# Kernel tuning notes

Hardware: AMD Instinct MI355X
Metric: run time of the kernel (lower is better)

## Reference

```python
import jax, jax.numpy as jnp
import numpy as np

S = 2048      # sequence length
E = 2048      # n_embd
H = 16        # n_head
D = E // H    # head_dim = 128
EPS = 1e-5


def _layer_norm(x, w):
    # eqx.nn.LayerNorm, use_bias=False: (x - mean) / sqrt(var + eps) * w
    mu = jnp.mean(x, axis=-1, keepdims=True)
    var = jnp.mean(jnp.square(x - mu), axis=-1, keepdims=True)
    return (x - mu) * jax.lax.rsqrt(var + EPS) * w


def setup_inputs() -> dict:
    key = jax.random.key(0)
    ks = jax.random.split(key, 7)
    x = jax.random.normal(ks[0], (S, E), dtype=jnp.float32)
    # equinox Linear weights are (out_features, in_features); y = W @ x
    w_attn = jax.random.normal(ks[1], (3 * E, E), dtype=jnp.float32) * 0.02
    w_proj_attn = jax.random.normal(ks[2], (E, E), dtype=jnp.float32) * 0.02
    w_fc = jax.random.normal(ks[3], (4 * E, E), dtype=jnp.float32) * 0.02
    w_proj_ffn = jax.random.normal(ks[4], (E, 4 * E), dtype=jnp.float32) * 0.02
    ln1_w = jnp.ones((E,), dtype=jnp.float32)
    ln2_w = jnp.ones((E,), dtype=jnp.float32)
    return {"x": x, "ln1_w": ln1_w, "ln2_w": ln2_w, "w_attn": w_attn,
            "w_proj_attn": w_proj_attn, "w_fc": w_fc, "w_proj_ffn": w_proj_ffn}


def reference(x, ln1_w, ln2_w, w_attn, w_proj_attn, w_fc, w_proj_ffn):
    # --- LN1 + fused QKV projection ---
    h = _layer_norm(x, ln1_w)                       # [S, E]
    qkv = h @ w_attn.T                              # [S, 3E]
    q, k, v = jnp.split(qkv, 3, axis=-1)
    q = q.reshape(S, H, D)
    k = k.reshape(S, H, D)
    v = v.reshape(S, H, D)
    # --- naive causal attention with materialized [H, S, T] scores ---
    scale = 1.0 / jnp.sqrt(jnp.float32(D))
    causal_bias = (jnp.arange(S)[:, None] < jnp.arange(S)[None, :]) * (-10000.0)
    scores = jnp.einsum('shd,thd->hst', q, k) * scale + causal_bias  # [H,S,T]
    probs = jax.nn.softmax(scores, axis=-1)
    attn = jnp.einsum('hst,thd->shd', probs, v).reshape(S, E)
    x = x + attn @ w_proj_attn.T
    # --- LN2 + GELU MLP ---
    h2 = _layer_norm(x, ln2_w)                      # [S, E]
    f = jax.nn.gelu(h2 @ w_fc.T) @ w_proj_ffn.T    # [S,4E] -> [S,E]
    return x + f
```

## Files before the change

### kernel.cpp

```cpp
#include <hip/hip_runtime.h>
#include <hip/hip_bf16.h>

#define S_LEN 2048
#define EMB   2048
#define NH    16
#define HD    128

typedef __bf16 bf16x8 __attribute__((ext_vector_type(8)));
typedef __bf16 bf16x4 __attribute__((ext_vector_type(4)));
typedef float  f32x4  __attribute__((ext_vector_type(4)));
typedef short  s16x4  __attribute__((ext_vector_type(4)));

__device__ __forceinline__ void async_copy16(void* lds, const void* g) {
  __builtin_amdgcn_global_load_lds((__attribute__((address_space(1))) void*)(void*)g,
                                   (__attribute__((address_space(3))) void*)lds, 16, 0, 0);
}

__device__ __forceinline__ unsigned lds_addr(const void* p) {
  return (unsigned)(uintptr_t)(const __attribute__((address_space(3))) char*)p;
}

__device__ __forceinline__ s16x4 tr16(unsigned addr) {
  s16x4 d;
  asm volatile("ds_read_b64_tr_b16 %0, %1" : "=v"(d) : "v"(addr));
  return d;
}

__device__ __forceinline__ float gelu_tanh(float x) {
  float x3 = x * x * x;
  float t  = 0.7978845608028654f * (x + 0.044715f * x3);
  float th = 1.0f - 2.0f / (__expf(2.0f * t) + 1.0f);
  return 0.5f * x * (1.0f + th);
}

__global__ __launch_bounds__(256) void cast_kernel(const float* __restrict__ in,
                                                   __bf16* __restrict__ out, int n) {
  int i = (blockIdx.x * 256 + threadIdx.x) * 4;
  if (i >= n) return;
  float4 v = *(const float4*)(in + i);
  bf16x4 o;
  o[0] = (__bf16)v.x; o[1] = (__bf16)v.y; o[2] = (__bf16)v.z; o[3] = (__bf16)v.w;
  *(bf16x4*)(out + i) = o;
}

__global__ __launch_bounds__(256) void ln_kernel(const float* __restrict__ x,
                                                 const float* __restrict__ w,
                                                 __bf16* __restrict__ out) {
  int row = blockIdx.x;
  int t = threadIdx.x;
  const float* xr = x + (size_t)row * EMB;
  float4 a = *(const float4*)(xr + t * 8);
  float4 b = *(const float4*)(xr + t * 8 + 4);
  float s  = a.x + a.y + a.z + a.w + b.x + b.y + b.z + b.w;
  float sq = a.x*a.x + a.y*a.y + a.z*a.z + a.w*a.w + b.x*b.x + b.y*b.y + b.z*b.z + b.w*b.w;
  #pragma unroll
  for (int o = 32; o > 0; o >>= 1) { s += __shfl_xor(s, o); sq += __shfl_xor(sq, o); }
  __shared__ float red[8];
  if ((t & 63) == 0) { red[t >> 6] = s; red[(t >> 6) + 4] = sq; }
  __syncthreads();
  s  = red[0] + red[1] + red[2] + red[3];
  sq = red[4] + red[5] + red[6] + red[7];
  float mu  = s * (1.0f / EMB);
  float var = sq * (1.0f / EMB) - mu * mu;
  float rs  = rsqrtf(var + 1e-5f);
  float4 w1 = *(const float4*)(w + t * 8);
  float4 w2 = *(const float4*)(w + t * 8 + 4);
  bf16x8 ov;
  ov[0] = (__bf16)((a.x - mu) * rs * w1.x);
  ov[1] = (__bf16)((a.y - mu) * rs * w1.y);
  ov[2] = (__bf16)((a.z - mu) * rs * w1.z);
  ov[3] = (__bf16)((a.w - mu) * rs * w1.w);
  ov[4] = (__bf16)((b.x - mu) * rs * w2.x);
  ov[5] = (__bf16)((b.y - mu) * rs * w2.y);
  ov[6] = (__bf16)((b.z - mu) * rs * w2.z);
  ov[7] = (__bf16)((b.w - mu) * rs * w2.w);
  *(bf16x8*)(out + (size_t)row * EMB + t * 8) = ov;
}

#define GPHASE(KH, MG, LOADB, STAGE_CALL, VMWAIT)                                           \
  {                                                                                         \
    if (LOADB) {                                                                            \
      _Pragma("unroll")                                                                     \
      for (int n = 0; n < 4; n++) {                                                         \
        int row = wc * 64 + n * 16 + fr;                                                    \
        b[n] = *(const bf16x8*)&Bs[((p * 2 + (KH)) * 256 + row) * 32 + ((g ^ (fr & 3)) << 3)]; \
      }                                                                                     \
    }                                                                                       \
    _Pragma("unroll")                                                                       \
    for (int m = 0; m < 4; m++) {                                                           \
      int row = wr * 128 + ((MG) * 4 + m) * 16 + fr;                                        \
      a[m] = *(const bf16x8*)&As[((p * 2 + (KH)) * 256 + row) * 32 + ((g ^ (fr & 3)) << 3)];   \
    }                                                                                       \
    STAGE_CALL;                                                                             \
    __builtin_amdgcn_sched_barrier(0);                                                      \
    __builtin_amdgcn_s_setprio(1);                                                          \
    _Pragma("unroll")                                                                       \
    for (int m = 0; m < 4; m++)                                                             \
      _Pragma("unroll")                                                                     \
      for (int n = 0; n < 4; n++)                                                           \
        acc[(MG) * 4 + m][n] =                                                              \
            __builtin_amdgcn_mfma_f32_16x16x32_bf16(a[m], b[n], acc[(MG) * 4 + m][n], 0, 0, 0); \
    __builtin_amdgcn_s_setprio(0);                                                          \
    VMWAIT;                                                                                 \
    __builtin_amdgcn_s_barrier();                                                           \
  }

template <int EPI>
__global__ __launch_bounds__(512, 2) void gemm256(const __bf16* __restrict__ A,
                                                  const __bf16* __restrict__ B,
                                                  void* __restrict__ Cv,
                                                  int M, int N, int K, int Ksl, int NN) {
  __shared__ __bf16 As[2 * 2 * 256 * 32];
  __shared__ __bf16 Bs[2 * 2 * 256 * 32];

  const int t = threadIdx.x, w = t >> 6, l = t & 63;
  const int fr = l & 15, g = l >> 4;
  const int wr = w >> 2, wc = w & 3;

  const int nwg = gridDim.x;
  const int wg = (blockIdx.x & 7) * (nwg >> 3) + (blockIdx.x >> 3);
  const int NMN = (M >> 8) * NN;
  const int z = wg / NMN, rr = wg - z * NMN;
  const int my = rr / NN, nx = rr - my * NN;
  const int m0 = my * 256, n0 = nx * 256;
  const int kb = z * Ksl;
  const int NT = Ksl >> 6;

  const int srow = t >> 2;
  const int schunk = (t & 3) ^ ((t >> 2) & 3);
  const __bf16* Abase = A + (size_t)(m0 + srow) * K + kb + schunk * 8;
  const __bf16* Bbase = B + (size_t)(n0 + srow) * K + kb + schunk * 8;
  const size_t K128 = (size_t)128 * K;
  __bf16* AsT = &As[t * 8];
  __bf16* BsT = &Bs[t * 8];

  auto stageA = [&](int pp, int kt2, int kh) {
    const __bf16* src = Abase + kt2 * 64 + kh * 32;
    __bf16* dst = AsT + (pp * 2 + kh) * 8192;
    async_copy16(dst, src);
    async_copy16(dst + 4096, src + K128);
  };
  auto stageB = [&](int pp, int kt2, int kh) {
    const __bf16* src = Bbase + kt2 * 64 + kh * 32;
    __bf16* dst = BsT + (pp * 2 + kh) * 8192;
    async_copy16(dst, src);
    async_copy16(dst + 4096, src + K128);
  };

  f32x4 acc[8][4] = {};

  stageA(0, 0, 0); stageB(0, 0, 0); stageA(0, 0, 1); stageB(0, 0, 1);
  asm volatile("s_waitcnt vmcnt(4)" ::: "memory");
  __builtin_amdgcn_s_barrier();

  for (int kt = 0; kt < NT; ++kt) {
    const int p = kt & 1, pn = p ^ 1;
    const bool pref = (kt + 1 < NT);
    bf16x8 a[4], b[4];
    GPHASE(0, 0, 1, if (pref) stageA(pn, kt + 1, 0), (void)0);
    GPHASE(0, 1, 0, if (pref) stageB(pn, kt + 1, 0),
           if (pref) { asm volatile("s_waitcnt vmcnt(4)" ::: "memory"); }
           else      { asm volatile("s_waitcnt vmcnt(0)" ::: "memory"); });
    GPHASE(1, 0, 1, if (pref) stageA(pn, kt + 1, 1), (void)0);
    GPHASE(1, 1, 0, if (pref) stageB(pn, kt + 1, 1),
           if (pref) { asm volatile("s_waitcnt vmcnt(4)" ::: "memory"); });
  }

  #pragma unroll
  for (int m = 0; m < 8; m++)
    #pragma unroll
    for (int n = 0; n < 4; n++)
      #pragma unroll
      for (int j = 0; j < 4; j++) {
        int orow = m0 + wr * 128 + m * 16 + g * 4 + j;
        int ocol = n0 + wc * 64 + n * 16 + fr;
        size_t idx = (size_t)orow * N + ocol;
        float v = acc[m][n][j];
        if (EPI == 0) {
          ((__bf16*)Cv)[idx] = (__bf16)v;
        } else if (EPI == 2) {
          ((__bf16*)Cv)[idx] = (__bf16)gelu_tanh(v);
        } else {
          atomicAdd((float*)Cv + idx, v);
        }
      }
}

__global__ __launch_bounds__(256) void attn_kernel(const __bf16* __restrict__ qkv,
                                                   __bf16* __restrict__ out) {
  __shared__ __bf16 Kt[2][64 * 128];
  __shared__ __bf16 Vt[2][64 * 128];
  __shared__ __bf16 Pb[4][16 * 64];

  const int bid = blockIdx.x;
  const int h = bid & 15;
  const int idx = bid >> 4;
  const int qb = (idx < 16) ? idx : 47 - idx;

  const int t = threadIdx.x, w = t >> 6, l = t & 63;
  const int g = l >> 4, fr = l & 15;
  const int fkb = g * 8;
  const int q0 = qb * 64 + w * 16;
  const float scale = 0.08838834764831845f;

  const int krow = w * 4 + g;
  const int kchunk = fr ^ (krow & 7);
  const int vkey = (l >> 1) & 3;
  const int vd0  = (l >> 3) * 16 + (l & 1) * 8;

  const size_t row3E = (size_t)(3 * EMB);
  const __bf16* Kg = qkv + EMB + h * HD;
  const __bf16* Vg = qkv + 2 * EMB + h * HD;

  bf16x8 qf[4];
  #pragma unroll
  for (int kc = 0; kc < 4; kc++)
    qf[kc] = *(const bf16x8*)&qkv[(size_t)(q0 + fr) * row3E + h * HD + kc * 32 + fkb];

  f32x4 o[8] = {};
  float mrun[4] = {-1e30f, -1e30f, -1e30f, -1e30f};
  float lsum[4] = {0.f, 0.f, 0.f, 0.f};

  const unsigned vtrb[2] = { lds_addr(&Vt[0][0]) + g * 2048 + fr * 8,
                             lds_addr(&Vt[1][0]) + g * 2048 + fr * 8 };

  auto stage = [&](int buf, int it) {
    const int t0 = it * 64;
    #pragma unroll
    for (int r = 0; r < 4; r++) {
      async_copy16(&Kt[buf][r * 2048 + w * 512],
                   Kg + (size_t)(t0 + r * 16 + krow) * row3E + kchunk * 8);
      async_copy16(&Vt[buf][(r * 4 + w) * 512],
                   Vg + (size_t)(t0 + r * 16 + w * 4 + vkey) * row3E + vd0);
    }
  };

  const int nt = qb + 1;
  stage(0, 0);
  int cur = 0;

  for (int it = 0; it < nt; it++) {
    __syncthreads();
    if (it + 1 < nt) stage(cur ^ 1, it + 1);
    const int t0 = it * 64;

    f32x4 s[4] = {};
    #pragma unroll
    for (int n = 0; n < 4; n++)
      #pragma unroll
      for (int kc = 0; kc < 4; kc++) {
        bf16x8 kf = *(const bf16x8*)&Kt[cur][(n * 16 + fr) * 128 +
                                            (((kc * 4 + g) ^ (fr & 7)) << 3)];
        s[n] = __builtin_amdgcn_mfma_f32_16x16x32_bf16(qf[kc], kf, s[n], 0, 0, 0);
      }
    #pragma unroll
    for (int n = 0; n < 4; n++)
      #pragma unroll
      for (int j = 0; j < 4; j++) {
        int tcol = t0 + n * 16 + fr;
        int qrow = q0 + g * 4 + j;
        float v = s[n][j] * scale;
        s[n][j] = (tcol > qrow) ? -1e30f : v;
      }
    float pm[4];
    #pragma unroll
    for (int j = 0; j < 4; j++) {
      pm[j] = fmaxf(fmaxf(s[0][j], s[1][j]), fmaxf(s[2][j], s[3][j]));
      #pragma unroll
      for (int off = 1; off < 16; off <<= 1) pm[j] = fmaxf(pm[j], __shfl_xor(pm[j], off));
    }
    float factor[4];
    #pragma unroll
    for (int j = 0; j < 4; j++) {
      float mn = fmaxf(mrun[j], pm[j]);
      factor[j] = __expf(mrun[j] - mn);
      mrun[j] = mn;
    }
    float rs[4] = {0.f, 0.f, 0.f, 0.f};
    #pragma unroll
    for (int n = 0; n < 4; n++)
      #pragma unroll
      for (int j = 0; j < 4; j++) {
        float p = __expf(s[n][j] - mrun[j]);
        s[n][j] = p;
        rs[j] += p;
      }
    #pragma unroll
    for (int j = 0; j < 4; j++) {
      #pragma unroll
      for (int off = 1; off < 16; off <<= 1) rs[j] += __shfl_xor(rs[j], off);
      lsum[j] = lsum[j] * factor[j] + rs[j];
    }
    #pragma unroll
    for (int b = 0; b < 8; b++)
      #pragma unroll
      for (int j = 0; j < 4; j++) o[b][j] *= factor[j];

    #pragma unroll
    for (int n = 0; n < 4; n++)
      #pragma unroll
      for (int j = 0; j < 4; j++) {
        int q   = g * 4 + j;
        int key = n * 16 + fr;
        int cs  = (key >> 3) ^ (q & 7);
        Pb[w][q * 64 + cs * 8 + (key & 7)] = (__bf16)s[n][j];
      }

    bf16x8 pf[2];
    #pragma unroll
    for (int kc = 0; kc < 2; kc++)
      pf[kc] = *(const bf16x8*)&Pb[w][fr * 64 + (((kc * 4 + g) ^ (fr & 7)) << 3)];

    const unsigned vtr = vtrb[cur];
    #pragma unroll
    for (int b = 0; b < 8; b++) {
      s16x4 t00 = tr16(vtr + b * 128);
      s16x4 t01 = tr16(vtr + b * 128 + 1024);
      s16x4 t10 = tr16(vtr + b * 128 + 8192);
      s16x4 t11 = tr16(vtr + b * 128 + 8192 + 1024);
      asm volatile("s_waitcnt lgkmcnt(0)");
      __builtin_amdgcn_sched_barrier(0);
      union { s16x4 hh[2]; bf16x8 v; } u0, u1;
      u0.hh[0] = t00; u0.hh[1] = t01;
      u1.hh[0] = t10; u1.hh[1] = t11;
      o[b] = __builtin_amdgcn_mfma_f32_16x16x32_bf16(pf[0], u0.v, o[b], 0, 0, 0);
      o[b] = __builtin_amdgcn_mfma_f32_16x16x32_bf16(pf[1], u1.v, o[b], 0, 0, 0);
    }
    cur ^= 1;
  }

  float rcp[4];
  #pragma unroll
  for (int j = 0; j < 4; j++) rcp[j] = 1.0f / lsum[j];
  #pragma unroll
  for (int b = 0; b < 8; b++)
    #pragma unroll
    for (int j = 0; j < 4; j++) {
      int qrow = q0 + g * 4 + j;
      out[(size_t)qrow * EMB + h * HD + b * 16 + fr] = (__bf16)(o[b][j] * rcp[j]);
    }
}

extern "C" void kernel_launch(void* const* d_in, const int* in_sizes, int n_in,
                              void* d_out, int out_size, void* d_ws, size_t ws_size,
                              hipStream_t stream) {
  const float* x     = (const float*)d_in[0];
  const float* ln1w  = (const float*)d_in[1];
  const float* ln2w  = (const float*)d_in[2];
  const float* wattn = (const float*)d_in[3];
  const float* wproja= (const float*)d_in[4];
  const float* wfc   = (const float*)d_in[5];
  const float* wprojf= (const float*)d_in[6];
  float* out = (float*)d_out;
  char* ws = (char*)d_ws;

  __bf16* wattn_b  = (__bf16*)(ws);
  __bf16* wproja_b = (__bf16*)(ws + 25165824);
  __bf16* wfc_b    = (__bf16*)(ws + 33554432);
  __bf16* wprojf_b = (__bf16*)(ws + 67108864);
  __bf16* h_b      = (__bf16*)(ws + 100663296);
  __bf16* qkv_b    = (__bf16*)(ws + 109051904);
  __bf16* attn_b   = (__bf16*)(ws + 134217728);
  __bf16* f1_b     = (__bf16*)(ws + 142606336);

  cast_kernel<<<12288, 256, 0, stream>>>(wattn,  wattn_b,  12582912);
  cast_kernel<<<4096,  256, 0, stream>>>(wproja, wproja_b, 4194304);
  cast_kernel<<<16384, 256, 0, stream>>>(wfc,    wfc_b,    16777216);
  cast_kernel<<<16384, 256, 0, stream>>>(wprojf, wprojf_b, 16777216);

  ln_kernel<<<S_LEN, 256, 0, stream>>>(x, ln1w, h_b);
  gemm256<0><<<192, 512, 0, stream>>>(h_b, wattn_b, qkv_b, S_LEN, 3 * EMB, EMB, EMB, 24);
  attn_kernel<<<dim3(512), 256, 0, stream>>>(qkv_b, attn_b);
  (void)hipMemcpyAsync(out, x, (size_t)S_LEN * EMB * sizeof(float), hipMemcpyDeviceToDevice, stream);
  gemm256<4><<<256, 512, 0, stream>>>(attn_b, wproja_b, out, S_LEN, EMB, EMB, EMB / 4, 8);
  ln_kernel<<<S_LEN, 256, 0, stream>>>(out, ln2w, h_b);
  gemm256<2><<<256, 512, 0, stream>>>(h_b, wfc_b, f1_b, S_LEN, 4 * EMB, EMB, EMB, 32);
  gemm256<4><<<256, 512, 0, stream>>>(f1_b, wprojf_b, out, S_LEN, EMB, 4 * EMB, 2048, 8);
}
```

Before: 468.8 us.

## Software-pipeline LDS fragment reads and deepen async prefetch in GEMM main loop

Restructures the GEMM k-loop so LDS fragment reads for the next MFMA phase are issued before the current phase's MFMAs, using double-buffered register fragments (aX/aY, bX/bY). Global-to-LDS prefetch now runs up to two half-tiles ahead with adjusted vmcnt waits, and the LDS swizzle pattern changes to a different XOR to cut bank conflicts. This aims to hide LDS read latency and global load latency behind matrix work. It costs more VGPRs for the extra fragment registers and makes the barrier and wait ordering more delicate.

```diff
diff --git a/kernel.cpp b/kernel.cpp
--- a/kernel.cpp
+++ b/kernel.cpp
@@ -77,33 +77,13 @@
   *(bf16x8*)(out + (size_t)row * EMB + t * 8) = ov;
 }
 
-#define GPHASE(KH, MG, LOADB, STAGE_CALL, VMWAIT)                                           \
-  {                                                                                         \
-    if (LOADB) {                                                                            \
-      _Pragma("unroll")                                                                     \
-      for (int n = 0; n < 4; n++) {                                                         \
-        int row = wc * 64 + n * 16 + fr;                                                    \
-        b[n] = *(const bf16x8*)&Bs[((p * 2 + (KH)) * 256 + row) * 32 + ((g ^ (fr & 3)) << 3)]; \
-      }                                                                                     \
-    }                                                                                       \
-    _Pragma("unroll")                                                                       \
-    for (int m = 0; m < 4; m++) {                                                           \
-      int row = wr * 128 + ((MG) * 4 + m) * 16 + fr;                                        \
-      a[m] = *(const bf16x8*)&As[((p * 2 + (KH)) * 256 + row) * 32 + ((g ^ (fr & 3)) << 3)];   \
-    }                                                                                       \
-    STAGE_CALL;                                                                             \
-    __builtin_amdgcn_sched_barrier(0);                                                      \
-    __builtin_amdgcn_s_setprio(1);                                                          \
-    _Pragma("unroll")                                                                       \
-    for (int m = 0; m < 4; m++)                                                             \
-      _Pragma("unroll")                                                                     \
-      for (int n = 0; n < 4; n++)                                                           \
-        acc[(MG) * 4 + m][n] =                                                              \
-            __builtin_amdgcn_mfma_f32_16x16x32_bf16(a[m], b[n], acc[(MG) * 4 + m][n], 0, 0, 0); \
-    __builtin_amdgcn_s_setprio(0);                                                          \
-    VMWAIT;                                                                                 \
-    __builtin_amdgcn_s_barrier();                                                           \
-  }
+#define MFMA16(AV, BV, MG)                                                                   \
+  _Pragma("unroll")                                                                          \
+  for (int m = 0; m < 4; m++)                                                                \
+    _Pragma("unroll")                                                                        \
+    for (int n = 0; n < 4; n++)                                                              \
+      acc[(MG) * 4 + m][n] =                                                                 \
+          __builtin_amdgcn_mfma_f32_16x16x32_bf16(AV[m], BV[n], acc[(MG) * 4 + m][n], 0, 0, 0);
 
 template <int EPI>
 __global__ __launch_bounds__(512, 2) void gemm256(const __bf16* __restrict__ A,
@@ -127,43 +107,84 @@
   const int NT = Ksl >> 6;
 
   const int srow = t >> 2;
-  const int schunk = (t & 3) ^ ((t >> 2) & 3);
+  const int schunk = (t & 3) ^ ((t >> 3) & 3);
   const __bf16* Abase = A + (size_t)(m0 + srow) * K + kb + schunk * 8;
   const __bf16* Bbase = B + (size_t)(n0 + srow) * K + kb + schunk * 8;
   const size_t K128 = (size_t)128 * K;
   __bf16* AsT = &As[t * 8];
   __bf16* BsT = &Bs[t * 8];
 
-  auto stageA = [&](int pp, int kt2, int kh) {
-    const __bf16* src = Abase + kt2 * 64 + kh * 32;
-    __bf16* dst = AsT + (pp * 2 + kh) * 8192;
+  auto stage = [&](const __bf16* base, __bf16* dstT, int kt, int kh) {
+    const __bf16* src = base + kt * 64 + kh * 32;
+    __bf16* dst = dstT + ((kt & 1) * 2 + kh) * 8192;
     async_copy16(dst, src);
     async_copy16(dst + 4096, src + K128);
   };
-  auto stageB = [&](int pp, int kt2, int kh) {
-    const __bf16* src = Bbase + kt2 * 64 + kh * 32;
-    __bf16* dst = BsT + (pp * 2 + kh) * 8192;
-    async_copy16(dst, src);
-    async_copy16(dst + 4096, src + K128);
+
+  const int gran = (g ^ ((fr >> 1) & 3)) << 3;
+  auto rdA = [&](bf16x8* dst, int kt, int kh, int mg) {
+    const int ub = ((kt & 1) * 2 + kh) * 256;
+    #pragma unroll
+    for (int m = 0; m < 4; m++) {
+      int row = wr * 128 + (mg * 4 + m) * 16 + fr;
+      dst[m] = *(const bf16x8*)&As[(ub + row) * 32 + gran];
+    }
   };
+  auto rdB = [&](bf16x8* dst, int kt, int kh) {
+    const int ub = ((kt & 1) * 2 + kh) * 256;
+    #pragma unroll
+    for (int n = 0; n < 4; n++) {
+      int row = wc * 64 + n * 16 + fr;
+      dst[n] = *(const bf16x8*)&Bs[(ub + row) * 32 + gran];
+    }
+  };
 
   f32x4 acc[8][4] = {};
-
-  stageA(0, 0, 0); stageB(0, 0, 0); stageA(0, 0, 1); stageB(0, 0, 1);
+  bf16x8 aX[4], aY[4], bX[4], bY[4];
+
+  stage(Abase, AsT, 0, 0); stage(Bbase, BsT, 0, 0);
+  stage(Abase, AsT, 0, 1); stage(Bbase, BsT, 0, 1);
+  if (1 < NT) { stage(Abase, AsT, 1, 0); stage(Bbase, BsT, 1, 0); }
   asm volatile("s_waitcnt vmcnt(4)" ::: "memory");
   __builtin_amdgcn_s_barrier();
+  rdB(bX, 0, 0);
+  rdA(aX, 0, 0, 0);
 
   for (int kt = 0; kt < NT; ++kt) {
-    const int p = kt & 1, pn = p ^ 1;
-    const bool pref = (kt + 1 < NT);
-    bf16x8 a[4], b[4];
-    GPHASE(0, 0, 1, if (pref) stageA(pn, kt + 1, 0), (void)0);
-    GPHASE(0, 1, 0, if (pref) stageB(pn, kt + 1, 0),
-           if (pref) { asm volatile("s_waitcnt vmcnt(4)" ::: "memory"); }
-           else      { asm volatile("s_waitcnt vmcnt(0)" ::: "memory"); });
-    GPHASE(1, 0, 1, if (pref) stageA(pn, kt + 1, 1), (void)0);
-    GPHASE(1, 1, 0, if (pref) stageB(pn, kt + 1, 1),
-           if (pref) { asm volatile("s_waitcnt vmcnt(4)" ::: "memory"); });
+    const bool s1 = (kt + 1 < NT), s2 = (kt + 2 < NT);
+    if (s1) stage(Abase, AsT, kt + 1, 1);
+    rdA(aY, kt, 0, 1);
+    __builtin_amdgcn_sched_barrier(0);
+    __builtin_amdgcn_s_setprio(1);
+    MFMA16(aX, bX, 0);
+    __builtin_amdgcn_s_setprio(0);
+    if (s2) { asm volatile("s_waitcnt vmcnt(6)" ::: "memory"); }
+    else    { asm volatile("s_waitcnt vmcnt(0)" ::: "memory"); }
+    __builtin_amdgcn_s_barrier();
+    if (s1) stage(Bbase, BsT, kt + 1, 1);
+    rdB(bY, kt, 1);
+    rdA(aX, kt, 1, 0);
+    __builtin_amdgcn_sched_barrier(0);
+    __builtin_amdgcn_s_setprio(1);
+    MFMA16(aY, bX, 1);
+    __builtin_amdgcn_s_setprio(0);
+    __builtin_amdgcn_s_barrier();
+    if (s2) stage(Abase, AsT, kt + 2, 0);
+    rdA(aY, kt, 1, 1);
+    __builtin_amdgcn_sched_barrier(0);
+    __builtin_amdgcn_s_setprio(1);
+    MFMA16(aX, bY, 0);
+    __builtin_amdgcn_s_setprio(0);
+    if (s2)      { asm volatile("s_waitcnt vmcnt(6)" ::: "memory"); }
+    else if (s1) { asm volatile("s_waitcnt vmcnt(0)" ::: "memory"); }
+    __builtin_amdgcn_s_barrier();
+    if (s2) stage(Bbase, BsT, kt + 2, 0);
+    if (s1) { rdB(bX, kt + 1, 0); rdA(aX, kt + 1, 0, 0); }
+    __builtin_amdgcn_sched_barrier(0);
+    __builtin_amdgcn_s_setprio(1);
+    MFMA16(aY, bY, 1);
+    __builtin_amdgcn_s_setprio(0);
+    __builtin_amdgcn_s_barrier();
   }
 
   #pragma unroll
```

Result: slower. 536.0 us (+14.3%).
